# Optimization experiments

Hardware: AMD Instinct MI355X
Metric: run time of the kernel (lower is better)

Reference implementation:

```python
import jax, jax.numpy as jnp
import numpy as np

F_BANKS = 8
D_IN = 592
FILTER_W = 5.0
BATCH = 8192


def _init(k, shape, fan_in):
    bound = 1.0 / np.sqrt(fan_in)
    return jax.random.uniform(k, shape, jnp.float32, -bound, bound)


def setup_inputs() -> dict:
    key = jax.random.key(0)
    ks = jax.random.split(key, 11)
    F = F_BANKS
    return {
        "x": jax.random.normal(ks[0], (BATCH, D_IN), jnp.float32),
        # per-bank Conv1d(1->3,k=3) and Conv1d(3->1,k=3), stacked over banks
        "conv1_w": _init(ks[1], (F, 3, 1, 3), 1 * 3),
        "conv1_b": _init(ks[2], (F, 3), 1 * 3),
        "conv2_w": _init(ks[3], (F, 1, 3, 3), 3 * 3),
        "conv2_b": _init(ks[4], (F, 1), 3 * 3),
        # per-bank MLP 36 -> 20 -> 10 -> 1
        "lin1_w": _init(ks[5], (F, 20, 36), 36),
        "lin1_b": _init(ks[6], (F, 20), 36),
        "lin2_w": _init(ks[7], (F, 10, 20), 20),
        "lin2_b": _init(ks[8], (F, 10), 20),
        "lin3_w": _init(ks[9], (F, 1, 10), 10),
        "lin3_b": _init(ks[10], (F, 1), 10),
    }


def _conv1d(x, w, b, stride):
    # x: [B, C_in, L], w: [C_out, C_in, K]
    y = jax.lax.conv_general_dilated(x, w, (stride,), "VALID",
                                     dimension_numbers=("NCH", "OIH", "NCH"))
    return y + b[None, :, None]


def _maxpool3s2(x):
    # MaxPool1d(kernel=3, stride=2) over last axis of [B, C, L]
    return jax.lax.reduce_window(x, -jnp.inf, jax.lax.max, (1, 1, 3), (1, 1, 2), "VALID")


def reference(x, conv1_w, conv1_b, conv2_w, conv2_b,
              lin1_w, lin1_b, lin2_w, lin2_b, lin3_w, lin3_b):
    B, D = x.shape
    f = jnp.arange(D, dtype=x.dtype)  # frequency grid [D]
    inv_2w2 = 1.0 / (2.0 * FILTER_W * FILTER_W)

    filtered_sum = jnp.zeros_like(x)
    H_list, xf_list, xs_list, f0_list = [], [], [], []
    for i in range(F_BANKS):
        x_aux = x - filtered_sum  # residual signal fed to bank i
        xs_list.append(x_aux)
        # conv bank: [B,1,592] -> [B,3,295] -> [B,3,147] -> [B,1,73] -> [B,1,36]
        h = x_aux[:, None, :]
        h = jax.nn.relu(_maxpool3s2(_conv1d(h, conv1_w[i], conv1_b[i], 2)))
        h = jax.nn.relu(_maxpool3s2(_conv1d(h, conv2_w[i], conv2_b[i], 2)))
        h = h[:, 0, :]  # squeeze(1) -> [B, 36]
        # linear bank: 36 -> 20 -> 10 -> 1 with sigmoid head
        h = jax.nn.relu(h @ lin1_w[i].T + lin1_b[i])
        h = jax.nn.relu(h @ lin2_w[i].T + lin2_b[i])
        h = jax.nn.sigmoid(h @ lin3_w[i].T + lin3_b[i])  # [B, 1]
        f0 = D * h  # center frequency per sample, [B, 1]
        # Gaussian filter per sample, vectorized over the batch (replaces per-row loop)
        H = jnp.exp(-jnp.square(f[None, :] - f0) * inv_2w2)  # [B, D]
        xf = x_aux * H
        filtered_sum = filtered_sum + xf
        H_list.append(H)
        xf_list.append(xf)
        f0_list.append(f0)
    return (jnp.stack(H_list), jnp.stack(xf_list), jnp.stack(xs_list), jnp.stack(f0_list))
```

## Files before the change

kernel.cpp:

```cpp
#include <hip/hip_runtime.h>
#include <math.h>

#define BATCH  8192
#define D_IN   592
#define FBANKS 8
#define P1     147
#define P2     36
#define NW     4

__global__ __launch_bounds__(256) void fb_kernel(
    const float* __restrict__ x,
    const float* __restrict__ c1w, const float* __restrict__ c1b,
    const float* __restrict__ c2w, const float* __restrict__ c2b,
    const float* __restrict__ l1w, const float* __restrict__ l1b,
    const float* __restrict__ l2w, const float* __restrict__ l2b,
    const float* __restrict__ l3w, const float* __restrict__ l3b,
    float* __restrict__ outH, float* __restrict__ outXF,
    float* __restrict__ outXS, float* __restrict__ outF0)
{
    __shared__ float s_c1w[72];
    __shared__ float s_c1b[24];
    __shared__ float s_c2w[72];
    __shared__ float s_c2b[8];
    __shared__ float s_l1w[5760];
    __shared__ float s_l1b[160];
    __shared__ float s_l2w[1600];
    __shared__ float s_l2b[80];
    __shared__ float s_l3w[80];
    __shared__ float s_l3b[8];
    __shared__ float s_xa[NW][D_IN];
    __shared__ float s_p1[NW][3][P1 + 1];
    __shared__ float s_p2[NW][P2];
    __shared__ float s_l1o[NW][20];
    __shared__ float s_l2o[NW][12];
    __shared__ float s_f0[NW];

    const int tid  = threadIdx.x;
    const int wave = tid >> 6;
    const int lane = tid & 63;
    const int row  = blockIdx.x * NW + wave;

    for (int i = tid; i < 72;   i += 256) s_c1w[i] = c1w[i];
    for (int i = tid; i < 24;   i += 256) s_c1b[i] = c1b[i];
    for (int i = tid; i < 72;   i += 256) s_c2w[i] = c2w[i];
    for (int i = tid; i < 8;    i += 256) s_c2b[i] = c2b[i];
    for (int i = tid; i < 5760; i += 256) s_l1w[i] = l1w[i];
    for (int i = tid; i < 160;  i += 256) s_l1b[i] = l1b[i];
    for (int i = tid; i < 1600; i += 256) s_l2w[i] = l2w[i];
    for (int i = tid; i < 80;   i += 256) s_l2b[i] = l2b[i];
    for (int i = tid; i < 80;   i += 256) s_l3w[i] = l3w[i];
    for (int i = tid; i < 8;    i += 256) s_l3b[i] = l3b[i];

    float* xa = s_xa[wave];
    for (int d = lane; d < D_IN; d += 64)
        xa[d] = x[(size_t)row * D_IN + d];
    __syncthreads();

    const float inv2w2 = 1.0f / (2.0f * 5.0f * 5.0f);

    for (int bank = 0; bank < FBANKS; ++bank) {
        float w1[3][3], b1[3], w2[3][3];
        #pragma unroll
        for (int c = 0; c < 3; ++c) {
            b1[c] = s_c1b[bank * 3 + c];
            #pragma unroll
            for (int k = 0; k < 3; ++k) {
                w1[c][k] = s_c1w[bank * 9 + c * 3 + k];
                w2[c][k] = s_c2w[bank * 9 + c * 3 + k];
            }
        }
        const float b2 = s_c2b[bank];

        for (int p = lane; p < P1; p += 64) {
            float xv[7];
            #pragma unroll
            for (int t = 0; t < 7; ++t) xv[t] = xa[4 * p + t];
            #pragma unroll
            for (int c = 0; c < 3; ++c) {
                float v0 = w1[c][0] * xv[0] + w1[c][1] * xv[1] + w1[c][2] * xv[2];
                float v1 = w1[c][0] * xv[2] + w1[c][1] * xv[3] + w1[c][2] * xv[4];
                float v2 = w1[c][0] * xv[4] + w1[c][1] * xv[5] + w1[c][2] * xv[6];
                float m  = fmaxf(fmaxf(v0, v1), v2) + b1[c];
                s_p1[wave][c][p] = fmaxf(m, 0.0f);
            }
        }
        __syncthreads();

        if (lane < P2) {
            const int q = lane;
            float vm[3];
            #pragma unroll
            for (int m = 0; m < 3; ++m) {
                float s = b2;
                #pragma unroll
                for (int c = 0; c < 3; ++c)
                    #pragma unroll
                    for (int k = 0; k < 3; ++k)
                        s += w2[c][k] * s_p1[wave][c][4 * q + 2 * m + k];
                vm[m] = s;
            }
            float mm = fmaxf(fmaxf(vm[0], vm[1]), vm[2]);
            s_p2[wave][q] = fmaxf(mm, 0.0f);
        }
        __syncthreads();

        if (lane < 20) {
            float acc = s_l1b[bank * 20 + lane];
            const float* wr = &s_l1w[bank * 720 + lane * 36];
            #pragma unroll
            for (int k = 0; k < 36; ++k) acc += wr[k] * s_p2[wave][k];
            s_l1o[wave][lane] = fmaxf(acc, 0.0f);
        }
        __syncthreads();

        if (lane < 10) {
            float acc = s_l2b[bank * 10 + lane];
            const float* wr = &s_l2w[bank * 200 + lane * 20];
            #pragma unroll
            for (int k = 0; k < 20; ++k) acc += wr[k] * s_l1o[wave][k];
            s_l2o[wave][lane] = fmaxf(acc, 0.0f);
        }
        __syncthreads();

        if (lane == 0) {
            float acc = s_l3b[bank];
            #pragma unroll
            for (int k = 0; k < 10; ++k)
                acc += s_l3w[bank * 10 + k] * s_l2o[wave][k];
            float sig = 1.0f / (1.0f + __expf(-acc));
            float f0  = (float)D_IN * sig;
            s_f0[wave] = f0;
            outF0[(size_t)bank * BATCH + row] = f0;
        }
        __syncthreads();

        const float f0 = s_f0[wave];
        const size_t base = ((size_t)bank * BATCH + row) * D_IN;
        for (int d = lane; d < D_IN; d += 64) {
            float xv = xa[d];
            float df = (float)d - f0;
            float Hv = __expf(-df * df * inv2w2);
            float xf = xv * Hv;
            outXS[base + d] = xv;
            outH[base + d]  = Hv;
            outXF[base + d] = xf;
            xa[d] = xv - xf;
        }
        __syncthreads();
    }
}

extern "C" void kernel_launch(void* const* d_in, const int* in_sizes, int n_in,
                              void* d_out, int out_size, void* d_ws, size_t ws_size,
                              hipStream_t stream) {
    const float* x   = (const float*)d_in[0];
    const float* c1w = (const float*)d_in[1];
    const float* c1b = (const float*)d_in[2];
    const float* c2w = (const float*)d_in[3];
    const float* c2b = (const float*)d_in[4];
    const float* l1w = (const float*)d_in[5];
    const float* l1b = (const float*)d_in[6];
    const float* l2w = (const float*)d_in[7];
    const float* l2b = (const float*)d_in[8];
    const float* l3w = (const float*)d_in[9];
    const float* l3b = (const float*)d_in[10];

    float* out = (float*)d_out;
    const size_t plane = (size_t)FBANKS * BATCH * D_IN;
    float* outH  = out;
    float* outXF = out + plane;
    float* outXS = out + 2 * plane;
    float* outF0 = out + 3 * plane;

    dim3 grid(BATCH / NW);
    dim3 block(256);
    fb_kernel<<<grid, block, 0, stream>>>(x, c1w, c1b, c2w, c2b,
                                          l1w, l1b, l2w, l2b, l3w, l3b,
                                          outH, outXF, outXS, outF0);
}
```

Baseline: 544.4 us.

## Replace block barriers with wave barriers and vectorize loads/stores with float4

```diff
diff --git a/kernel.cpp b/kernel.cpp
--- a/kernel.cpp
+++ b/kernel.cpp
@@ -6,7 +6,10 @@
 #define FBANKS 8
 #define P1     147
 #define P2     36
+#define P1PAD  152
 #define NW     4
+
+#define WAVE_SYNC() do { __builtin_amdgcn_wave_barrier(); asm volatile("" ::: "memory"); } while (0)
 
 __global__ __launch_bounds__(256) void fb_kernel(
     const float* __restrict__ x,
@@ -18,22 +21,20 @@
     float* __restrict__ outH, float* __restrict__ outXF,
     float* __restrict__ outXS, float* __restrict__ outF0)
 {
-    __shared__ float s_c1w[72];
-    __shared__ float s_c1b[24];
-    __shared__ float s_c2w[72];
-    __shared__ float s_c2b[8];
-    __shared__ float s_l1w[5760];
-    __shared__ float s_l1b[160];
-    __shared__ float s_l2w[1600];
-    __shared__ float s_l2b[80];
-    __shared__ float s_l3w[80];
-    __shared__ float s_l3b[8];
-    __shared__ float s_xa[NW][D_IN];
-    __shared__ float s_p1[NW][3][P1 + 1];
-    __shared__ float s_p2[NW][P2];
-    __shared__ float s_l1o[NW][20];
-    __shared__ float s_l2o[NW][12];
-    __shared__ float s_f0[NW];
+    __shared__ __align__(16) float s_c1w[72];
+    __shared__ __align__(16) float s_c1b[24];
+    __shared__ __align__(16) float s_c2w[72];
+    __shared__ __align__(16) float s_c2b[8];
+    __shared__ __align__(16) float s_l1b[160];
+    __shared__ __align__(16) float s_l2w[1600];
+    __shared__ __align__(16) float s_l2b[80];
+    __shared__ __align__(16) float s_l3w[80];
+    __shared__ __align__(16) float s_l3b[8];
+    __shared__ __align__(16) float s_xa[NW][D_IN];
+    __shared__ __align__(16) float s_p1[NW][3][P1PAD];
+    __shared__ __align__(16) float s_p2[NW][40];
+    __shared__ __align__(16) float s_l1o[NW][20];
+    __shared__ __align__(16) float s_l2o[NW][12];
 
     const int tid  = threadIdx.x;
     const int wave = tid >> 6;
@@ -44,7 +45,6 @@
     for (int i = tid; i < 24;   i += 256) s_c1b[i] = c1b[i];
     for (int i = tid; i < 72;   i += 256) s_c2w[i] = c2w[i];
     for (int i = tid; i < 8;    i += 256) s_c2b[i] = c2b[i];
-    for (int i = tid; i < 5760; i += 256) s_l1w[i] = l1w[i];
     for (int i = tid; i < 160;  i += 256) s_l1b[i] = l1b[i];
     for (int i = tid; i < 1600; i += 256) s_l2w[i] = l2w[i];
     for (int i = tid; i < 80;   i += 256) s_l2b[i] = l2b[i];
@@ -52,8 +52,13 @@
     for (int i = tid; i < 8;    i += 256) s_l3b[i] = l3b[i];
 
     float* xa = s_xa[wave];
-    for (int d = lane; d < D_IN; d += 64)
-        xa[d] = x[(size_t)row * D_IN + d];
+    {
+        const float* xrow = x + (size_t)row * D_IN;
+        for (int i = lane; i < 148; i += 64) {
+            float4 v = *(const float4*)&xrow[4 * i];
+            *(float4*)&xa[4 * i] = v;
+        }
+    }
     __syncthreads();
 
     const float inv2w2 = 1.0f / (2.0f * 5.0f * 5.0f);
@@ -72,81 +77,99 @@
         const float b2 = s_c2b[bank];
 
         for (int p = lane; p < P1; p += 64) {
-            float xv[7];
-            #pragma unroll
-            for (int t = 0; t < 7; ++t) xv[t] = xa[4 * p + t];
+            float4 a = *(const float4*)&xa[4 * p];
+            float4 b = *(const float4*)&xa[4 * p + 4];
+            float xv0 = a.x, xv1 = a.y, xv2 = a.z, xv3 = a.w;
+            float xv4 = b.x, xv5 = b.y, xv6 = b.z;
             #pragma unroll
             for (int c = 0; c < 3; ++c) {
-                float v0 = w1[c][0] * xv[0] + w1[c][1] * xv[1] + w1[c][2] * xv[2];
-                float v1 = w1[c][0] * xv[2] + w1[c][1] * xv[3] + w1[c][2] * xv[4];
-                float v2 = w1[c][0] * xv[4] + w1[c][1] * xv[5] + w1[c][2] * xv[6];
+                float v0 = w1[c][0] * xv0 + w1[c][1] * xv1 + w1[c][2] * xv2;
+                float v1 = w1[c][0] * xv2 + w1[c][1] * xv3 + w1[c][2] * xv4;
+                float v2 = w1[c][0] * xv4 + w1[c][1] * xv5 + w1[c][2] * xv6;
                 float m  = fmaxf(fmaxf(v0, v1), v2) + b1[c];
                 s_p1[wave][c][p] = fmaxf(m, 0.0f);
             }
         }
-        __syncthreads();
+        WAVE_SYNC();
 
         if (lane < P2) {
             const int q = lane;
-            float vm[3];
-            #pragma unroll
-            for (int m = 0; m < 3; ++m) {
-                float s = b2;
-                #pragma unroll
-                for (int c = 0; c < 3; ++c)
-                    #pragma unroll
-                    for (int k = 0; k < 3; ++k)
-                        s += w2[c][k] * s_p1[wave][c][4 * q + 2 * m + k];
-                vm[m] = s;
-            }
-            float mm = fmaxf(fmaxf(vm[0], vm[1]), vm[2]);
+            float acc0 = b2, acc1 = b2, acc2 = b2;
+            #pragma unroll
+            for (int c = 0; c < 3; ++c) {
+                const float* r = s_p1[wave][c];
+                float4 a = *(const float4*)&r[4 * q];
+                float4 b = *(const float4*)&r[4 * q + 4];
+                float v0 = a.x, v1 = a.y, v2 = a.z, v3 = a.w, v4 = b.x, v5 = b.y, v6 = b.z;
+                acc0 += w2[c][0] * v0 + w2[c][1] * v1 + w2[c][2] * v2;
+                acc1 += w2[c][0] * v2 + w2[c][1] * v3 + w2[c][2] * v4;
+                acc2 += w2[c][0] * v4 + w2[c][1] * v5 + w2[c][2] * v6;
+            }
+            float mm = fmaxf(fmaxf(acc0, acc1), acc2);
             s_p2[wave][q] = fmaxf(mm, 0.0f);
         }
-        __syncthreads();
+        WAVE_SYNC();
 
         if (lane < 20) {
+            const float4* wr = (const float4*)(l1w + bank * 720 + lane * 36);
             float acc = s_l1b[bank * 20 + lane];
-            const float* wr = &s_l1w[bank * 720 + lane * 36];
-            #pragma unroll
-            for (int k = 0; k < 36; ++k) acc += wr[k] * s_p2[wave][k];
+            #pragma unroll
+            for (int k = 0; k < 9; ++k) {
+                float4 w = wr[k];
+                float4 v = *(const float4*)&s_p2[wave][4 * k];
+                acc += w.x * v.x + w.y * v.y + w.z * v.z + w.w * v.w;
+            }
             s_l1o[wave][lane] = fmaxf(acc, 0.0f);
         }
-        __syncthreads();
+        WAVE_SYNC();
 
         if (lane < 10) {
+            const float4* wr = (const float4*)&s_l2w[bank * 200 + lane * 20];
             float acc = s_l2b[bank * 10 + lane];
-            const float* wr = &s_l2w[bank * 200 + lane * 20];
-            #pragma unroll
-            for (int k = 0; k < 20; ++k) acc += wr[k] * s_l1o[wave][k];
+            #pragma unroll
+            for (int k = 0; k < 5; ++k) {
+                float4 w = wr[k];
+                float4 v = *(const float4*)&s_l1o[wave][4 * k];
+                acc += w.x * v.x + w.y * v.y + w.z * v.z + w.w * v.w;
+            }
             s_l2o[wave][lane] = fmaxf(acc, 0.0f);
         }
-        __syncthreads();
-
+        WAVE_SYNC();
+
+        float f0v = 0.0f;
         if (lane == 0) {
             float acc = s_l3b[bank];
             #pragma unroll
             for (int k = 0; k < 10; ++k)
                 acc += s_l3w[bank * 10 + k] * s_l2o[wave][k];
             float sig = 1.0f / (1.0f + __expf(-acc));
-            float f0  = (float)D_IN * sig;
-            s_f0[wave] = f0;
-            outF0[(size_t)bank * BATCH + row] = f0;
-        }
-        __syncthreads();
-
-        const float f0 = s_f0[wave];
+            f0v = (float)D_IN * sig;
+            outF0[(size_t)bank * BATCH + row] = f0v;
+        }
+        f0v = __shfl(f0v, 0);
+
         const size_t base = ((size_t)bank * BATCH + row) * D_IN;
-        for (int d = lane; d < D_IN; d += 64) {
-            float xv = xa[d];
-            float df = (float)d - f0;
-            float Hv = __expf(-df * df * inv2w2);
-            float xf = xv * Hv;
-            outXS[base + d] = xv;
-            outH[base + d]  = Hv;
-            outXF[base + d] = xf;
-            xa[d] = xv - xf;
-        }
-        __syncthreads();
+        for (int i = lane; i < 148; i += 64) {
+            float4 xv = *(const float4*)&xa[4 * i];
+            float d0 = (float)(4 * i)     - f0v;
+            float d1 = (float)(4 * i + 1) - f0v;
+            float d2 = (float)(4 * i + 2) - f0v;
+            float d3 = (float)(4 * i + 3) - f0v;
+            float4 Hv, xf, xn;
+            Hv.x = __expf(-d0 * d0 * inv2w2);
+            Hv.y = __expf(-d1 * d1 * inv2w2);
+            Hv.z = __expf(-d2 * d2 * inv2w2);
+            Hv.w = __expf(-d3 * d3 * inv2w2);
+            xf.x = xv.x * Hv.x;  xf.y = xv.y * Hv.y;
+            xf.z = xv.z * Hv.z;  xf.w = xv.w * Hv.w;
+            xn.x = xv.x - xf.x;  xn.y = xv.y - xf.y;
+            xn.z = xv.z - xf.z;  xn.w = xv.w - xf.w;
+            *(float4*)&outXS[base + 4 * i] = xv;
+            *(float4*)&outH [base + 4 * i] = Hv;
+            *(float4*)&outXF[base + 4 * i] = xf;
+            *(float4*)&xa[4 * i] = xn;
+        }
+        WAVE_SYNC();
     }
 }
 
```

New measurement: 499.0 us. 1.09x faster.
